# Optimization experiments

Hardware: AMD Instinct MI355X
Metric: run time of the kernel (lower is better)

The kernel has to match this reference:

```python
import jax, jax.numpy as jnp
import numpy as np

B, S, T = 2, 1024, 1024          # batch, new tokens, cache length (prefill: S == T)
DIM, NH, NKV, HD = 2048, 16, 4, 128
FFN = 5632
EPS = 1e-5
STD = 0.02


def rms_norm(x, w, eps=EPS):
    return x * jax.lax.rsqrt(jnp.mean(x * x, axis=-1, keepdims=True) + eps) * w


def apply_rope(x, freqs_cis):
    # x: [B, S, H, HD]; freqs_cis: [S, HD//2, 2] (cos, sin) over consecutive pairs
    xr = x.reshape(*x.shape[:-1], HD // 2, 2)
    cos = freqs_cis[None, :, None, :, 0]
    sin = freqs_cis[None, :, None, :, 1]
    x0, x1 = xr[..., 0], xr[..., 1]
    rot = jnp.stack([x0 * cos - x1 * sin, x0 * sin + x1 * cos], axis=-1)
    return rot.reshape(x.shape)


def setup_inputs() -> dict:
    key = jax.random.key(0)
    ks = jax.random.split(key, 10)
    x = jax.random.normal(ks[0], (B, S, DIM), jnp.float32)
    # rotary tables
    inv_freq = 1.0 / (10000.0 ** (np.arange(0, HD, 2, dtype=np.float32) / HD))
    ang = np.outer(np.arange(S, dtype=np.float32), inv_freq)          # [S, HD//2]
    freqs_cis = jnp.asarray(np.stack([np.cos(ang), np.sin(ang)], -1), jnp.float32)
    cache_k = jnp.zeros((1, B, T, NKV, HD), jnp.float32)
    cache_v = jnp.zeros((1, B, T, NKV, HD), jnp.float32)
    mask = jnp.triu(jnp.full((S, T), -1e9, jnp.float32), k=1)         # additive causal
    wq = jax.random.normal(ks[1], (DIM, NH, HD), jnp.float32) * STD
    wk = jax.random.normal(ks[2], (DIM, NKV, HD), jnp.float32) * STD
    wv = jax.random.normal(ks[3], (DIM, NKV, HD), jnp.float32) * STD
    wo = jax.random.normal(ks[4], (NH * HD, DIM), jnp.float32) * STD
    w_gate = jax.random.normal(ks[5], (DIM, FFN), jnp.float32) * STD
    w_up = jax.random.normal(ks[6], (DIM, FFN), jnp.float32) * STD
    w_down = jax.random.normal(ks[7], (FFN, DIM), jnp.float32) * STD
    attn_norm_w = jnp.ones((DIM,), jnp.float32)
    ffn_norm_w = jnp.ones((DIM,), jnp.float32)
    return dict(x=x, freqs_cis=freqs_cis, cache_k=cache_k, cache_v=cache_v,
                mask=mask, wq=wq, wk=wk, wv=wv, wo=wo, w_gate=w_gate,
                w_up=w_up, w_down=w_down, attn_norm_w=attn_norm_w,
                ffn_norm_w=ffn_norm_w, layer_idx=0)


def reference(x, freqs_cis, cache_k, cache_v, mask, wq, wk, wv, wo,
              w_gate, w_up, w_down, attn_norm_w, ffn_norm_w, layer_idx):
    # --- attention sub-block ---
    h = rms_norm(x, attn_norm_w)
    q = jnp.einsum('bsd,dhk->bshk', h, wq)          # [B,S,NH,HD]
    k = jnp.einsum('bsd,dgk->bsgk', h, wk)          # [B,S,NKV,HD]
    v = jnp.einsum('bsd,dgk->bsgk', h, wv)
    q = apply_rope(q, freqs_cis)
    k = apply_rope(k, freqs_cis)
    # append to per-layer KV cache at position 0 (prefill)
    cache_k = jax.lax.dynamic_update_slice(cache_k, k[None], (layer_idx, 0, 0, 0, 0))
    cache_v = jax.lax.dynamic_update_slice(cache_v, v[None], (layer_idx, 0, 0, 0, 0))
    keys = cache_k[layer_idx]                        # [B,T,NKV,HD]
    vals = cache_v[layer_idx]
    J = NH // NKV                                    # query heads per kv head
    qg = q.reshape(B, S, NKV, J, HD)
    scale = 1.0 / jnp.sqrt(jnp.float32(HD))
    scores = jnp.einsum('bsgjd,btgd->bgjst', qg, keys) * scale  # [B,NKV,J,S,T]
    scores = scores + mask                           # broadcast [S,T]
    probs = jax.nn.softmax(scores, axis=-1)
    ctx = jnp.einsum('bgjst,btgd->bsgjd', probs, vals).reshape(B, S, NH * HD)
    x = x + ctx @ wo
    # --- SwiGLU FFN sub-block ---
    hf = rms_norm(x, ffn_norm_w)
    ffn = (jax.nn.silu(hf @ w_gate) * (hf @ w_up)) @ w_down
    x = x + ffn
    return (x, cache_k, cache_v)
```

## Files before the change

kernel.cpp:

```cpp
#include <hip/hip_runtime.h>

typedef float f32x4 __attribute__((ext_vector_type(4)));
typedef __bf16 bf16x8 __attribute__((ext_vector_type(8)));
typedef unsigned short u16;

#define DIM 2048
#define SEQ 1024
#define BSZ 2
#define NH 16
#define NKV 4
#define HD 128
#define FFNDIM 5632
#define MROWS (BSZ * SEQ)

__device__ __forceinline__ u16 f2bf(float f) {
  union { float f; unsigned u; } v; v.f = f;
  unsigned u = v.u;
  unsigned r = (u + 0x7fffu + ((u >> 16) & 1u)) >> 16;
  return (u16)r;
}
__device__ __forceinline__ float bf2f(u16 h) {
  union { unsigned u; float f; } v; v.u = ((unsigned)h) << 16; return v.f;
}

__device__ __forceinline__ void gld16(const void* g, void* l) {
  __builtin_amdgcn_global_load_lds(
      (const __attribute__((address_space(1))) unsigned int*)g,
      (__attribute__((address_space(3))) unsigned int*)l, 16, 0, 0);
}

__global__ __launch_bounds__(256) void kxpose(const float* __restrict__ W,
                                              u16* __restrict__ Wt,
                                              int K, int N, int rs, int ro) {
  __shared__ float t[64][65];
  int kb = blockIdx.y * 64, nb = blockIdx.x * 64;
  int tid = threadIdx.x;
#pragma unroll
  for (int it = 0; it < 16; ++it) {
    int idx = it * 256 + tid;
    int r = idx >> 6, c = idx & 63;
    t[r][c] = W[(size_t)(kb + r) * N + nb + c];
  }
  __syncthreads();
#pragma unroll
  for (int it = 0; it < 16; ++it) {
    int idx = it * 256 + tid;
    int rn = idx >> 6, ck = idx & 63;
    Wt[((size_t)(nb + rn) * rs + ro) * K + kb + ck] = f2bf(t[ck][rn]);
  }
}

__global__ __launch_bounds__(256) void kvxpose(const u16* __restrict__ v,
                                               u16* __restrict__ vt) {
  __shared__ u16 t[64][66];
  int bg = blockIdx.z;
  int b = bg >> 2, g = bg & 3;
  int s0 = blockIdx.x * 64, d0 = blockIdx.y * 64;
  int tid = threadIdx.x;
  int rr = tid >> 4, cc = (tid & 15) * 4;
#pragma unroll
  for (int it = 0; it < 4; ++it) {
    int r = it * 16 + rr;
    *(uint2*)&t[r][cc] =
        *(const uint2*)(v + (size_t)(b * SEQ + s0 + r) * (NKV * HD) + g * HD + d0 + cc);
  }
  __syncthreads();
#pragma unroll
  for (int it = 0; it < 4; ++it) {
    int r = it * 16 + rr;
    u16 o[4] = {t[cc][r], t[cc + 1][r], t[cc + 2][r], t[cc + 3][r]};
    *(uint2*)(vt + (size_t)((b * NKV + g) * HD + d0 + r) * SEQ + s0 + cc) = *(const uint2*)o;
  }
}

__global__ __launch_bounds__(256) void krmsnorm(const float* __restrict__ x,
                                                const float* __restrict__ w,
                                                u16* __restrict__ out) {
  int row = blockIdx.x, tid = threadIdx.x;
  const float* xr = x + (size_t)row * DIM;
  float4 a = *(const float4*)(xr + tid * 8);
  float4 b = *(const float4*)(xr + tid * 8 + 4);
  float ss = a.x * a.x + a.y * a.y + a.z * a.z + a.w * a.w +
             b.x * b.x + b.y * b.y + b.z * b.z + b.w * b.w;
#pragma unroll
  for (int off = 1; off < 64; off <<= 1) ss += __shfl_xor(ss, off, 64);
  __shared__ float red[4];
  if ((tid & 63) == 0) red[tid >> 6] = ss;
  __syncthreads();
  float tot = red[0] + red[1] + red[2] + red[3];
  float sc = rsqrtf(tot * (1.0f / DIM) + 1e-5f);
  float xs[8] = {a.x, a.y, a.z, a.w, b.x, b.y, b.z, b.w};
  const float* wr = w + tid * 8;
  u16 o[8];
#pragma unroll
  for (int j = 0; j < 8; ++j) o[j] = f2bf(xs[j] * sc * wr[j]);
  *(int4*)(out + (size_t)row * DIM + tid * 8) = *(const int4*)o;
}

__global__ __launch_bounds__(256) void krope_q(u16* __restrict__ q,
                                               const float* __restrict__ fc) {
  int t = blockIdx.x * 256 + threadIdx.x;
  int j = t & 63;
  int h = (t >> 6) & (NH - 1);
  int row = t >> 10;
  int s = row & (SEQ - 1);
  size_t off = (size_t)row * DIM + h * HD + 2 * j;
  unsigned pk = *(unsigned*)(q + off);
  float x0 = bf2f((u16)pk), x1 = bf2f((u16)(pk >> 16));
  float cs = fc[s * HD + 2 * j], sn = fc[s * HD + 2 * j + 1];
  float y0 = x0 * cs - x1 * sn;
  float y1 = x0 * sn + x1 * cs;
  *(unsigned*)(q + off) = (unsigned)f2bf(y0) | ((unsigned)f2bf(y1) << 16);
}

__global__ __launch_bounds__(256) void krope_k(u16* __restrict__ k,
                                               const float* __restrict__ fc,
                                               float* __restrict__ ck) {
  int t = blockIdx.x * 256 + threadIdx.x;
  int j = t & 63;
  int g = (t >> 6) & (NKV - 1);
  int row = t >> 8;
  int s = row & (SEQ - 1);
  size_t off = (size_t)row * (NKV * HD) + g * HD + 2 * j;
  unsigned pk = *(unsigned*)(k + off);
  float x0 = bf2f((u16)pk), x1 = bf2f((u16)(pk >> 16));
  float cs = fc[s * HD + 2 * j], sn = fc[s * HD + 2 * j + 1];
  float y0 = x0 * cs - x1 * sn;
  float y1 = x0 * sn + x1 * cs;
  *(unsigned*)(k + off) = (unsigned)f2bf(y0) | ((unsigned)f2bf(y1) << 16);
  ck[off] = y0;
  ck[off + 1] = y1;
}

template <int EPI>
__global__ __launch_bounds__(512, 4) void kgemm(
    const u16* __restrict__ A, const u16* __restrict__ Bt, int N, int K,
    u16* o0, u16* __restrict__ o1, u16* __restrict__ o2,
    float* of, const float* res) {
  __shared__ u16 As[2][128 * 64];
  __shared__ u16 Bs[2][128 * 64];
  int bn = blockIdx.x * 128, bm = blockIdx.y * 128;
  int tid = threadIdx.x, lane = tid & 63, wv = tid >> 6;
  int wm = (wv >> 2) * 64;
  int wn = (wv & 3) * 32;
  int r16 = lane & 15, grp = lane >> 4;
  int srow = lane >> 3;
  int schunk = ((lane & 7) ^ srow) * 8;
  f32x4 acc[4][2] = {};
  const u16* Abase = A + (size_t)(bm + wv * 16) * K + schunk;
  const u16* Bbase = Bt + (size_t)(bn + wv * 16) * K + schunk;
  int woff = wv * 16 * 64;

  auto STAGE = [&](int buf, int k0) {
#pragma unroll
    for (int j = 0; j < 2; ++j) {
      gld16(Abase + (size_t)(j * 8 + srow) * K + k0, &As[buf][woff + j * 512]);
      gld16(Bbase + (size_t)(j * 8 + srow) * K + k0, &Bs[buf][woff + j * 512]);
    }
  };
  auto COMPUTE = [&](int buf) {
#pragma unroll
    for (int kk = 0; kk < 2; ++kk) {
      int swz = (((kk << 2) | grp) ^ (r16 & 7)) * 8;
      bf16x8 af[4], bfr[2];
#pragma unroll
      for (int m = 0; m < 4; ++m)
        af[m] = *(const bf16x8*)&As[buf][(wm + m * 16 + r16) * 64 + swz];
#pragma unroll
      for (int n = 0; n < 2; ++n)
        bfr[n] = *(const bf16x8*)&Bs[buf][(wn + n * 16 + r16) * 64 + swz];
#pragma unroll
      for (int m = 0; m < 4; ++m)
#pragma unroll
        for (int n = 0; n < 2; ++n)
          acc[m][n] = __builtin_amdgcn_mfma_f32_16x16x32_bf16(af[m], bfr[n], acc[m][n], 0, 0, 0);
    }
  };

  STAGE(0, 0);
  int nt = K >> 6;
  for (int t = 0; t < nt; ++t) {
    int cur = t & 1;
    if (t + 1 < nt) {
      STAGE(cur ^ 1, (t + 1) << 6);
      asm volatile("s_waitcnt vmcnt(4)" ::: "memory");
    } else {
      asm volatile("s_waitcnt vmcnt(0)" ::: "memory");
    }
    __builtin_amdgcn_sched_barrier(0);
    __builtin_amdgcn_s_barrier();
    __builtin_amdgcn_sched_barrier(0);
    COMPUTE(cur);
    __builtin_amdgcn_s_barrier();
  }

#pragma unroll
  for (int mi = 0; mi < 4; ++mi) {
#pragma unroll
    for (int ni = 0; ni < 2; ++ni) {
#pragma unroll
      for (int r = 0; r < 4; ++r) {
        int gr = bm + wm + mi * 16 + grp * 4 + r;
        int gc = bn + wn + ni * 16 + r16;
        float v = acc[mi][ni][r];
        if constexpr (EPI == 0) {
          if (gc < DIM) {
            o0[(size_t)gr * DIM + gc] = f2bf(v);
          } else if (gc < DIM + 512) {
            o1[(size_t)gr * 512 + (gc - DIM)] = f2bf(v);
          } else {
            int c2 = gc - (DIM + 512);
            of[(size_t)gr * 512 + c2] = v;
            o2[(size_t)gr * 512 + c2] = f2bf(v);
          }
        } else {
          of[(size_t)gr * N + gc] = v + res[(size_t)gr * N + gc];
        }
      }
    }
  }
}

__global__ __launch_bounds__(512, 4) void kgemm_gu(
    const u16* __restrict__ A, const u16* __restrict__ Bt,
    u16* __restrict__ out) {
  const int K = DIM;
  __shared__ u16 As[2][128 * 64];
  __shared__ u16 Bs[2][128 * 64];
  int bn = blockIdx.x * 128, bm = blockIdx.y * 128;
  int tid = threadIdx.x, lane = tid & 63, wv = tid >> 6;
  int wm = (wv >> 2) * 64;
  int wn = (wv & 3) * 32;
  int r16 = lane & 15, grp = lane >> 4;
  int srow = lane >> 3;
  int schunk = ((lane & 7) ^ srow) * 8;
  f32x4 acc[4][2] = {};
  const u16* Abase = A + (size_t)(bm + wv * 16) * K + schunk;
  const u16* Bbase = Bt + (size_t)(bn + wv * 16) * K + schunk;
  int woff = wv * 16 * 64;

  auto STAGE = [&](int buf, int k0) {
#pragma unroll
    for (int j = 0; j < 2; ++j) {
      gld16(Abase + (size_t)(j * 8 + srow) * K + k0, &As[buf][woff + j * 512]);
      gld16(Bbase + (size_t)(j * 8 + srow) * K + k0, &Bs[buf][woff + j * 512]);
    }
  };
  auto COMPUTE = [&](int buf) {
#pragma unroll
    for (int kk = 0; kk < 2; ++kk) {
      int swz = (((kk << 2) | grp) ^ (r16 & 7)) * 8;
      bf16x8 af[4], bfr[2];
#pragma unroll
      for (int m = 0; m < 4; ++m)
        af[m] = *(const bf16x8*)&As[buf][(wm + m * 16 + r16) * 64 + swz];
#pragma unroll
      for (int n = 0; n < 2; ++n)
        bfr[n] = *(const bf16x8*)&Bs[buf][(wn + n * 16 + r16) * 64 + swz];
#pragma unroll
      for (int m = 0; m < 4; ++m)
#pragma unroll
        for (int n = 0; n < 2; ++n)
          acc[m][n] = __builtin_amdgcn_mfma_f32_16x16x32_bf16(af[m], bfr[n], acc[m][n], 0, 0, 0);
    }
  };

  STAGE(0, 0);
  int nt = K >> 6;
  for (int t = 0; t < nt; ++t) {
    int cur = t & 1;
    if (t + 1 < nt) {
      STAGE(cur ^ 1, (t + 1) << 6);
      asm volatile("s_waitcnt vmcnt(4)" ::: "memory");
    } else {
      asm volatile("s_waitcnt vmcnt(0)" ::: "memory");
    }
    __builtin_amdgcn_sched_barrier(0);
    __builtin_amdgcn_s_barrier();
    __builtin_amdgcn_sched_barrier(0);
    COMPUTE(cur);
    __builtin_amdgcn_s_barrier();
  }

  bool evenlane = (r16 & 1) == 0;
#pragma unroll
  for (int mi = 0; mi < 4; ++mi) {
#pragma unroll
    for (int ni = 0; ni < 2; ++ni) {
#pragma unroll
      for (int r = 0; r < 4; ++r) {
        float v = acc[mi][ni][r];
        float pv = __shfl_xor(v, 1, 64);
        if (evenlane) {
          int gr = bm + wm + mi * 16 + grp * 4 + r;
          int gc = bn + wn + ni * 16 + r16;
          float sg = v / (1.0f + __expf(-v));
          out[(size_t)gr * FFNDIM + (gc >> 1)] = f2bf(sg * pv);
        }
      }
    }
  }
}

__global__ __launch_bounds__(256) void kattn(const u16* __restrict__ qb,
                                             const u16* __restrict__ kb,
                                             const u16* __restrict__ vtb,
                                             u16* __restrict__ ctxb) {
  __shared__ u16 Ks[2][64 * 128];
  __shared__ u16 Vs[2][128 * 64];
  __shared__ u16 Plds[4][16][72];
  int tid = threadIdx.x;
  int l = tid & 63, wv = tid >> 6;
  int qg = 15 - blockIdx.x;
  int h = blockIdx.y, b = blockIdx.z;
  int g = h >> 2;
  int q0 = qg * 64 + wv * 16;
  int r16 = l & 15, grp = l >> 4;
  const float scale = 0.08838834764831845f;
  bf16x8 qf[4];
  {
    const u16* qrow = qb + (size_t)(b * SEQ + q0 + r16) * DIM + h * HD + grp * 8;
#pragma unroll
    for (int c = 0; c < 4; ++c) qf[c] = *(const bf16x8*)(qrow + c * 32);
  }
  const u16* kg = kb + (size_t)b * SEQ * (NKV * HD) + g * HD;
  const u16* vg = vtb + (size_t)((b * NKV + g) * HD) * SEQ;

  auto STAGE = [&](int buf, int t0) {
#pragma unroll
    for (int p = 0; p < 4; ++p) {
      int row = p * 16 + wv * 4 + (l >> 4);
      int ch = (l & 15) ^ (row & 7);
      gld16(kg + (size_t)(t0 + row) * (NKV * HD) + ch * 8,
            &Ks[buf][p * 2048 + wv * 512]);
    }
#pragma unroll
    for (int p = 0; p < 4; ++p) {
      int row = p * 32 + wv * 8 + (l >> 3);
      int ch = (l & 7) ^ (row & 7);
      gld16(vg + (size_t)row * SEQ + t0 + ch * 8,
            &Vs[buf][p * 2048 + wv * 512]);
    }
  };

  f32x4 ctx[8] = {};
  float m = -1e30f, lsum = 0.0f;
  int q_idx = q0 + r16;
  int ntiles = qg + 1;

  STAGE(0, 0);
  for (int tt = 0; tt < ntiles; ++tt) {
    int cur = tt & 1;
    if (tt + 1 < ntiles) {
      STAGE(cur ^ 1, (tt + 1) * 64);
      asm volatile("s_waitcnt vmcnt(8)" ::: "memory");
    } else {
      asm volatile("s_waitcnt vmcnt(0)" ::: "memory");
    }
    __builtin_amdgcn_sched_barrier(0);
    __builtin_amdgcn_s_barrier();
    __builtin_amdgcn_sched_barrier(0);
    int t0 = tt * 64;
    f32x4 d[4] = {{0.f, 0.f, 0.f, 0.f}, {0.f, 0.f, 0.f, 0.f},
                  {0.f, 0.f, 0.f, 0.f}, {0.f, 0.f, 0.f, 0.f}};
    __builtin_amdgcn_s_setprio(1);
#pragma unroll
    for (int c = 0; c < 4; ++c) {
#pragma unroll
      for (int ch = 0; ch < 4; ++ch) {
        int row = ch * 16 + r16;
        bf16x8 kf = *(const bf16x8*)&Ks[cur][row * 128 + (((c * 4 + grp) ^ (row & 7)) * 8)];
        d[ch] = __builtin_amdgcn_mfma_f32_16x16x32_bf16(kf, qf[c], d[ch], 0, 0, 0);
      }
    }
    __builtin_amdgcn_s_setprio(0);
    float p[16];
    float mx = -1e30f;
#pragma unroll
    for (int ch = 0; ch < 4; ++ch) {
#pragma unroll
      for (int r = 0; r < 4; ++r) {
        int tA = t0 + ch * 16 + grp * 4 + r;
        float s = d[ch][r] * scale;
        if (tA > q_idx) s = -1e30f;
        p[ch * 4 + r] = s;
        mx = fmaxf(mx, s);
      }
    }
    mx = fmaxf(mx, __shfl_xor(mx, 16, 64));
    mx = fmaxf(mx, __shfl_xor(mx, 32, 64));
    if (!__all(mx - m <= 8.0f)) {
      float mnew = fmaxf(m, mx);
      float corr = __expf(m - mnew);
      lsum *= corr;
      float cf[4];
#pragma unroll
      for (int r = 0; r < 4; ++r) cf[r] = __shfl(corr, grp * 4 + r, 64);
#pragma unroll
      for (int dc = 0; dc < 8; ++dc)
#pragma unroll
        for (int r = 0; r < 4; ++r) ctx[dc][r] *= cf[r];
      m = mnew;
    }
    float psum = 0.f;
#pragma unroll
    for (int i = 0; i < 16; ++i) {
      p[i] = __expf(p[i] - m);
      psum += p[i];
    }
    psum += __shfl_xor(psum, 16, 64);
    psum += __shfl_xor(psum, 32, 64);
    lsum += psum;
#pragma unroll
    for (int ch = 0; ch < 4; ++ch) {
      unsigned w0 = (unsigned)f2bf(p[ch * 4]) | ((unsigned)f2bf(p[ch * 4 + 1]) << 16);
      unsigned w1 = (unsigned)f2bf(p[ch * 4 + 2]) | ((unsigned)f2bf(p[ch * 4 + 3]) << 16);
      *(unsigned*)&Plds[wv][r16][ch * 16 + grp * 4] = w0;
      *(unsigned*)&Plds[wv][r16][ch * 16 + grp * 4 + 2] = w1;
    }
    bf16x8 pa0, pa1;
    {
      union { bf16x8 v; int4 q; } u0, u1;
      u0.q = *(const int4*)&Plds[wv][r16][grp * 8];
      u1.q = *(const int4*)&Plds[wv][r16][32 + grp * 8];
      pa0 = u0.v;
      pa1 = u1.v;
    }
    __builtin_amdgcn_s_setprio(1);
#pragma unroll
    for (int dc = 0; dc < 8; ++dc) {
      int row = dc * 16 + r16;
      bf16x8 vf0 = *(const bf16x8*)&Vs[cur][row * 64 + ((grp ^ (row & 7)) * 8)];
      bf16x8 vf1 = *(const bf16x8*)&Vs[cur][row * 64 + (((grp + 4) ^ (row & 7)) * 8)];
      ctx[dc] = __builtin_amdgcn_mfma_f32_16x16x32_bf16(pa0, vf0, ctx[dc], 0, 0, 0);
      ctx[dc] = __builtin_amdgcn_mfma_f32_16x16x32_bf16(pa1, vf1, ctx[dc], 0, 0, 0);
    }
    __builtin_amdgcn_s_setprio(0);
    __builtin_amdgcn_s_barrier();
  }
  float linv = 1.0f / lsum;
  float lf[4];
#pragma unroll
  for (int r = 0; r < 4; ++r) lf[r] = __shfl(linv, grp * 4 + r, 64);
  u16* crow = ctxb + (size_t)(b * SEQ + q0) * DIM + h * HD;
#pragma unroll
  for (int dc = 0; dc < 8; ++dc)
#pragma unroll
    for (int r = 0; r < 4; ++r)
      crow[(size_t)(grp * 4 + r) * DIM + dc * 16 + r16] = f2bf(ctx[dc][r] * lf[r]);
}

extern "C" void kernel_launch(void* const* d_in, const int* in_sizes, int n_in,
                              void* d_out, int out_size, void* d_ws, size_t ws_size,
                              hipStream_t stream) {
  const float* x = (const float*)d_in[0];
  const float* fc = (const float*)d_in[1];
  const float* wq = (const float*)d_in[5];
  const float* wk = (const float*)d_in[6];
  const float* wv = (const float*)d_in[7];
  const float* wo = (const float*)d_in[8];
  const float* wg = (const float*)d_in[9];
  const float* wu = (const float*)d_in[10];
  const float* wd = (const float*)d_in[11];
  const float* anw = (const float*)d_in[12];
  const float* fnw = (const float*)d_in[13];

  float* out_x = (float*)d_out;
  float* out_ck = out_x + (size_t)MROWS * DIM;
  float* out_cv = out_ck + (size_t)MROWS * NKV * HD;

  char* ws = (char*)d_ws;
  u16* h_b    = (u16*)(ws);
  u16* q_b    = (u16*)(ws + (8u << 20));
  u16* k_b    = (u16*)(ws + (16u << 20));
  u16* v_b    = (u16*)(ws + (18u << 20));
  u16* ctx_b  = (u16*)(ws + (20u << 20));
  u16* hf_b   = (u16*)(ws + (28u << 20));
  u16* Wt     = (u16*)(ws + (60u << 20));
  u16* vt_b   = h_b;
  u16* Wt_gu  = (u16*)(ws + (36u << 20));
  u16* g_b    = (u16*)(ws);
  u16* Wt_dn  = (u16*)(ws + (36u << 20));

  kxpose<<<dim3(2048 / 64, 2048 / 64), 256, 0, stream>>>(wq, Wt, 2048, 2048, 1, 0);
  kxpose<<<dim3(512 / 64, 2048 / 64), 256, 0, stream>>>(wk, Wt + (size_t)2048 * 2048, 2048, 512, 1, 0);
  kxpose<<<dim3(512 / 64, 2048 / 64), 256, 0, stream>>>(wv, Wt + (size_t)2560 * 2048, 2048, 512, 1, 0);

  krmsnorm<<<MROWS, 256, 0, stream>>>(x, anw, h_b);
  kgemm<0><<<dim3(3072 / 128, 16), 512, 0, stream>>>(h_b, Wt, 3072, 2048,
                                                     q_b, k_b, v_b, out_cv, nullptr);
  krope_q<<<8192, 256, 0, stream>>>(q_b, fc);
  krope_k<<<2048, 256, 0, stream>>>(k_b, fc, out_ck);
  kvxpose<<<dim3(SEQ / 64, HD / 64, BSZ * NKV), 256, 0, stream>>>(v_b, vt_b);
  kattn<<<dim3(SEQ / 64, NH, BSZ), 256, 0, stream>>>(q_b, k_b, vt_b, ctx_b);

  kxpose<<<dim3(32, 32), 256, 0, stream>>>(wo, Wt, 2048, 2048, 1, 0);
  kgemm<2><<<dim3(16, 16), 512, 0, stream>>>(ctx_b, Wt, 2048, 2048,
                                             nullptr, nullptr, nullptr, out_x, x);
  krmsnorm<<<MROWS, 256, 0, stream>>>(out_x, fnw, hf_b);

  kxpose<<<dim3(5632 / 64, 2048 / 64), 256, 0, stream>>>(wg, Wt_gu, 2048, 5632, 2, 0);
  kxpose<<<dim3(5632 / 64, 2048 / 64), 256, 0, stream>>>(wu, Wt_gu, 2048, 5632, 2, 1);
  kgemm_gu<<<dim3(11264 / 128, 16), 512, 0, stream>>>(hf_b, Wt_gu, g_b);
  kxpose<<<dim3(2048 / 64, 5632 / 64), 256, 0, stream>>>(wd, Wt_dn, 5632, 2048, 1, 0);
  kgemm<2><<<dim3(16, 16), 512, 0, stream>>>(g_b, Wt_dn, 2048, 5632,
                                             nullptr, nullptr, nullptr, out_x, out_x);
}
```

Baseline: 387.0 us.

## Fuse RoPE into QKV GEMM epilogue and add XCD-aware block swizzle

Removes the separate rope_q and rope_k kernels and applies the rotary embedding inside the QKV GEMM epilogue. Each lane gets its pair partner through a lane shuffle and writes both the bf16 K and the fp32 cache_k directly. The GEMM kernels also remap block indices in groups of 8, likely to spread tiles across XCDs for L2 locality. This saves two launches and a read-modify-write pass over Q and K, at the cost of extra epilogue work and reuse of the res pointer as the cache_k output.

New measurement: 399.0 us. +3.1%, slower.

```diff
diff --git a/kernel.cpp b/kernel.cpp
--- a/kernel.cpp
+++ b/kernel.cpp
@@ -97,49 +97,18 @@
   *(int4*)(out + (size_t)row * DIM + tid * 8) = *(const int4*)o;
 }
 
-__global__ __launch_bounds__(256) void krope_q(u16* __restrict__ q,
-                                               const float* __restrict__ fc) {
-  int t = blockIdx.x * 256 + threadIdx.x;
-  int j = t & 63;
-  int h = (t >> 6) & (NH - 1);
-  int row = t >> 10;
-  int s = row & (SEQ - 1);
-  size_t off = (size_t)row * DIM + h * HD + 2 * j;
-  unsigned pk = *(unsigned*)(q + off);
-  float x0 = bf2f((u16)pk), x1 = bf2f((u16)(pk >> 16));
-  float cs = fc[s * HD + 2 * j], sn = fc[s * HD + 2 * j + 1];
-  float y0 = x0 * cs - x1 * sn;
-  float y1 = x0 * sn + x1 * cs;
-  *(unsigned*)(q + off) = (unsigned)f2bf(y0) | ((unsigned)f2bf(y1) << 16);
-}
-
-__global__ __launch_bounds__(256) void krope_k(u16* __restrict__ k,
-                                               const float* __restrict__ fc,
-                                               float* __restrict__ ck) {
-  int t = blockIdx.x * 256 + threadIdx.x;
-  int j = t & 63;
-  int g = (t >> 6) & (NKV - 1);
-  int row = t >> 8;
-  int s = row & (SEQ - 1);
-  size_t off = (size_t)row * (NKV * HD) + g * HD + 2 * j;
-  unsigned pk = *(unsigned*)(k + off);
-  float x0 = bf2f((u16)pk), x1 = bf2f((u16)(pk >> 16));
-  float cs = fc[s * HD + 2 * j], sn = fc[s * HD + 2 * j + 1];
-  float y0 = x0 * cs - x1 * sn;
-  float y1 = x0 * sn + x1 * cs;
-  *(unsigned*)(k + off) = (unsigned)f2bf(y0) | ((unsigned)f2bf(y1) << 16);
-  ck[off] = y0;
-  ck[off + 1] = y1;
-}
-
 template <int EPI>
 __global__ __launch_bounds__(512, 4) void kgemm(
     const u16* __restrict__ A, const u16* __restrict__ Bt, int N, int K,
     u16* o0, u16* __restrict__ o1, u16* __restrict__ o2,
-    float* of, const float* res) {
+    float* of, const float* res, const float* __restrict__ fc) {
   __shared__ u16 As[2][128 * 64];
   __shared__ u16 Bs[2][128 * 64];
-  int bn = blockIdx.x * 128, bm = blockIdx.y * 128;
+  int nwg = gridDim.x * gridDim.y;
+  int lin = blockIdx.y * gridDim.x + blockIdx.x;
+  int cpx = nwg >> 3;
+  int swzb = (lin & 7) * cpx + (lin >> 3);
+  int bn = (swzb % gridDim.x) * 128, bm = (swzb / gridDim.x) * 128;
   int tid = threadIdx.x, lane = tid & 63, wv = tid >> 6;
   int wm = (wv >> 2) * 64;
   int wn = (wv & 3) * 32;
@@ -194,6 +163,7 @@
     __builtin_amdgcn_s_barrier();
   }
 
+  bool oddlane = (r16 & 1) != 0;
 #pragma unroll
   for (int mi = 0; mi < 4; ++mi) {
 #pragma unroll
@@ -204,10 +174,22 @@
         int gc = bn + wn + ni * 16 + r16;
         float v = acc[mi][ni][r];
         if constexpr (EPI == 0) {
-          if (gc < DIM) {
-            o0[(size_t)gr * DIM + gc] = f2bf(v);
-          } else if (gc < DIM + 512) {
-            o1[(size_t)gr * 512 + (gc - DIM)] = f2bf(v);
+          float pv = __shfl_xor(v, 1, 64);
+          if (gc < DIM + 512) {
+            int s_idx = gr & (SEQ - 1);
+            int jp = (gc & 127) >> 1;
+            float2 cs = *(const float2*)(fc + s_idx * HD + jp * 2);
+            float y;
+            if (oddlane) y = pv * cs.y + v * cs.x;
+            else         y = v * cs.x - pv * cs.y;
+            if (gc < DIM) {
+              o0[(size_t)gr * DIM + gc] = f2bf(y);
+            } else {
+              int c2 = gc - DIM;
+              o1[(size_t)gr * 512 + c2] = f2bf(y);
+              res ? (void)0 : (void)0;
+              ((float*)res)[(size_t)gr * 512 + c2] = y;
+            }
           } else {
             int c2 = gc - (DIM + 512);
             of[(size_t)gr * 512 + c2] = v;
@@ -227,7 +209,11 @@
   const int K = DIM;
   __shared__ u16 As[2][128 * 64];
   __shared__ u16 Bs[2][128 * 64];
-  int bn = blockIdx.x * 128, bm = blockIdx.y * 128;
+  int nwg = gridDim.x * gridDim.y;
+  int lin = blockIdx.y * gridDim.x + blockIdx.x;
+  int cpx = nwg >> 3;
+  int swzb = (lin & 7) * cpx + (lin >> 3);
+  int bn = (swzb % gridDim.x) * 128, bm = (swzb / gridDim.x) * 128;
   int tid = threadIdx.x, lane = tid & 63, wv = tid >> 6;
   int wm = (wv >> 2) * 64;
   int wn = (wv & 3) * 32;
@@ -488,15 +474,13 @@
 
   krmsnorm<<<MROWS, 256, 0, stream>>>(x, anw, h_b);
   kgemm<0><<<dim3(3072 / 128, 16), 512, 0, stream>>>(h_b, Wt, 3072, 2048,
-                                                     q_b, k_b, v_b, out_cv, nullptr);
-  krope_q<<<8192, 256, 0, stream>>>(q_b, fc);
-  krope_k<<<2048, 256, 0, stream>>>(k_b, fc, out_ck);
+                                                     q_b, k_b, v_b, out_cv, out_ck, fc);
   kvxpose<<<dim3(SEQ / 64, HD / 64, BSZ * NKV), 256, 0, stream>>>(v_b, vt_b);
   kattn<<<dim3(SEQ / 64, NH, BSZ), 256, 0, stream>>>(q_b, k_b, vt_b, ctx_b);
 
   kxpose<<<dim3(32, 32), 256, 0, stream>>>(wo, Wt, 2048, 2048, 1, 0);
   kgemm<2><<<dim3(16, 16), 512, 0, stream>>>(ctx_b, Wt, 2048, 2048,
-                                             nullptr, nullptr, nullptr, out_x, x);
+                                             nullptr, nullptr, nullptr, out_x, x, nullptr);
   krmsnorm<<<MROWS, 256, 0, stream>>>(out_x, fnw, hf_b);
 
   kxpose<<<dim3(5632 / 64, 2048 / 64), 256, 0, stream>>>(wg, Wt_gu, 2048, 5632, 2, 0);
@@ -504,5 +488,5 @@
   kgemm_gu<<<dim3(11264 / 128, 16), 512, 0, stream>>>(hf_b, Wt_gu, g_b);
   kxpose<<<dim3(2048 / 64, 5632 / 64), 256, 0, stream>>>(wd, Wt_dn, 5632, 2048, 1, 0);
   kgemm<2><<<dim3(16, 16), 512, 0, stream>>>(g_b, Wt_dn, 2048, 5632,
-                                             nullptr, nullptr, nullptr, out_x, out_x);
-}
+                                             nullptr, nullptr, nullptr, out_x, out_x, nullptr);
+}
```
